# Performance work log

Measured on AMD Instinct MI355X. Metric: run time of the kernel, lower is better.

Reference implementation:

```python
import jax, jax.numpy as jnp
import numpy as np

D_MODEL = 512
NUM_FACTORS = 32
SCALE = D_MODEL ** 0.5


def setup_inputs() -> dict:
    key = jax.random.key(0)
    ks = jax.random.split(key, 12)
    B, T, TF = 64, 1024, 512
    s = 0.02
    return {
        "y_hat": jax.random.normal(ks[0], (B, T, D_MODEL), jnp.float32),
        "weather_hist": jax.random.normal(ks[1], (B, T, NUM_FACTORS), jnp.float32),
        "weather_fore": jax.random.normal(ks[2], (B, TF, NUM_FACTORS), jnp.float32),
        "Wq": jax.random.normal(ks[3], (D_MODEL, D_MODEL), jnp.float32) * s,
        "bq": jnp.zeros((D_MODEL,), jnp.float32),
        "Wk": jax.random.normal(ks[4], (NUM_FACTORS, D_MODEL), jnp.float32) * s,
        "bk": jnp.zeros((D_MODEL,), jnp.float32),
        "Wv": jax.random.normal(ks[5], (NUM_FACTORS, D_MODEL), jnp.float32) * s,
        "bv": jnp.zeros((D_MODEL,), jnp.float32),
        "Ws": jax.random.normal(ks[6], (D_MODEL, D_MODEL), jnp.float32) * s,
        "bs": jnp.zeros((D_MODEL,), jnp.float32),
    }


def reference(y_hat, weather_hist, weather_fore, Wq, bq, Wk, bk, Wv, bv, Ws, bs):
    # weather: [B, S, F] with S = T_hist + T_fore
    weather = jnp.concatenate([weather_hist, weather_fore], axis=1)
    Q = y_hat @ Wq + bq                         # [B, T, D]
    K = weather @ Wk + bk                       # [B, S, D]
    V = weather @ Wv + bv                       # [B, S, D]
    scores = jnp.einsum("btd,bsd->bts", Q, K) / SCALE
    attn = jax.nn.softmax(scores, axis=-1)      # [B, T, S]
    correction = jnp.einsum("bts,bsd->btd", attn, V)
    combined = correction @ Ws + bs             # [B, T, D]
    # pooled softmax gating over time
    logits = jnp.sum(combined * y_hat, axis=-1, keepdims=True) / SCALE  # [B, T, 1]
    P = jax.nn.softmax(logits, axis=1)
    final = jnp.sum(P * y_hat, axis=1, keepdims=True)  # [B, 1, D]
    return y_hat + final  # broadcast = expand_as
```

## Files before the change

kernel.cpp:

```cpp
#include <hip/hip_runtime.h>
#include <hip/hip_bf16.h>

typedef __bf16 bf16_t;
typedef bf16_t bf16x8 __attribute__((ext_vector_type(8)));
typedef bf16_t bf16x4 __attribute__((ext_vector_type(4)));
typedef float  floatx4 __attribute__((ext_vector_type(4)));

#define MFMA16(a,b,c) __builtin_amdgcn_mfma_f32_16x16x32_bf16((a),(b),(c),0,0,0)

constexpr float INV_SCALE = 0.04419417382415922f;

__device__ __forceinline__ bf16x8 load8(const void* p, size_t idx, int isbf) {
    if (isbf) return *(const bf16x8*)((const bf16_t*)p + idx);
    const floatx4* f = (const floatx4*)((const float*)p + idx);
    floatx4 a = f[0], b = f[1];
    bf16x8 r;
    r[0]=(bf16_t)a[0]; r[1]=(bf16_t)a[1]; r[2]=(bf16_t)a[2]; r[3]=(bf16_t)a[3];
    r[4]=(bf16_t)b[0]; r[5]=(bf16_t)b[1]; r[6]=(bf16_t)b[2]; r[7]=(bf16_t)b[3];
    return r;
}
__device__ __forceinline__ float loadf(const void* p, size_t idx, int isbf) {
    return isbf ? (float)((const bf16_t*)p)[idx] : ((const float*)p)[idx];
}

__global__ __launch_bounds__(256) void k_detect(
    const void* __restrict__ y, int* __restrict__ flag,
    const void* __restrict__ bq, const void* __restrict__ bv,
    const void* __restrict__ bs,
    float* __restrict__ bqf, float* __restrict__ bvf, float* __restrict__ bsf)
{
    __shared__ int cnt[4];
    const unsigned* w = (const unsigned*)y;
    unsigned x = w[threadIdx.x];
    unsigned e = (x >> 7) & 0xFFu;
    bool hit = (e >= 100u && e <= 141u);
    unsigned long long m = __ballot(hit);
    if ((threadIdx.x & 63) == 0) cnt[threadIdx.x >> 6] = __popcll(m);
    __syncthreads();
    int isbf = (cnt[0] + cnt[1] + cnt[2] + cnt[3]) >= 128;
    if (threadIdx.x == 0) *flag = isbf;
    for (int i = threadIdx.x; i < 512; i += 256) {
        bqf[i] = loadf(bq, i, isbf);
        bvf[i] = loadf(bv, i, isbf);
        bsf[i] = loadf(bs, i, isbf);
    }
}

__global__ __launch_bounds__(256) void k_wtrans(
    const void* __restrict__ Ws, bf16_t* __restrict__ WsT,
    const int* __restrict__ flag)
{
    int isbf = *flag;
    int idx = blockIdx.x * 256 + threadIdx.x;
    int k = idx >> 9, n = idx & 511;
    WsT[(size_t)n * 512 + k] = (bf16_t)loadf(Ws, idx, isbf);
}

__global__ __launch_bounds__(256) void k_m12(
    const void* __restrict__ Wq, const void* __restrict__ Wk,
    const void* __restrict__ Wv, const bf16_t* __restrict__ WsT,
    const float* __restrict__ bqf, const float* __restrict__ bvf,
    const float* __restrict__ bsf,
    bf16_t* __restrict__ M1, bf16_t* __restrict__ M2,
    float* __restrict__ b2, float* __restrict__ bqk,
    const int* __restrict__ flag)
{
    int isbf = *flag;
    if (blockIdx.x == 0) {
        int wave = threadIdx.x >> 6, lane = threadIdx.x & 63;
        int u = lane & 15, q = lane >> 4;
        int n0 = wave * 128;
        {
            floatx4 acc[2][8] = {};
            for (int ks = 0; ks < 16; ++ks) {
                bf16x8 a0 = load8(Wk, (size_t)u * 512 + ks * 32 + q * 8, isbf);
                bf16x8 a1 = load8(Wk, (size_t)(16 + u) * 512 + ks * 32 + q * 8, isbf);
#pragma unroll
                for (int nt = 0; nt < 8; ++nt) {
                    bf16x8 bb = load8(Wq, (size_t)(n0 + nt * 16 + u) * 512 + ks * 32 + q * 8, isbf);
                    acc[0][nt] = MFMA16(a0, bb, acc[0][nt]);
                    acc[1][nt] = MFMA16(a1, bb, acc[1][nt]);
                }
            }
#pragma unroll
            for (int mt = 0; mt < 2; ++mt)
#pragma unroll
                for (int nt = 0; nt < 8; ++nt)
#pragma unroll
                    for (int r = 0; r < 4; ++r)
                        M1[(size_t)(mt * 16 + q * 4 + r) * 512 + n0 + nt * 16 + u] =
                            (bf16_t)acc[mt][nt][r];
        }
        {
            floatx4 acc[2][8] = {};
            for (int ks = 0; ks < 16; ++ks) {
                bf16x8 a0 = load8(Wv, (size_t)u * 512 + ks * 32 + q * 8, isbf);
                bf16x8 a1 = load8(Wv, (size_t)(16 + u) * 512 + ks * 32 + q * 8, isbf);
#pragma unroll
                for (int nt = 0; nt < 8; ++nt) {
                    bf16x8 bb = *(const bf16x8*)(WsT + (size_t)(n0 + nt * 16 + u) * 512 + ks * 32 + q * 8);
                    acc[0][nt] = MFMA16(a0, bb, acc[0][nt]);
                    acc[1][nt] = MFMA16(a1, bb, acc[1][nt]);
                }
            }
#pragma unroll
            for (int mt = 0; mt < 2; ++mt)
#pragma unroll
                for (int nt = 0; nt < 8; ++nt)
#pragma unroll
                    for (int r = 0; r < 4; ++r)
                        M2[(size_t)(mt * 16 + q * 4 + r) * 512 + n0 + nt * 16 + u] =
                            (bf16_t)acc[mt][nt][r];
        }
    } else if (blockIdx.x <= 2) {
        int n = (blockIdx.x - 1) * 256 + threadIdx.x;
        float s = 0.f;
        for (int d = 0; d < 512; ++d) s += bvf[d] * (float)WsT[(size_t)n * 512 + d];
        b2[n] = s + bsf[n];
    } else {
        if (threadIdx.x < 32) {
            int f = threadIdx.x;
            float s = 0.f;
            for (int d = 0; d < 512; ++d) s += bqf[d] * loadf(Wk, (size_t)f * 512 + d, isbf);
            bqk[f] = s;
        }
    }
}

__global__ __launch_bounds__(256) void k_weather(
    const void* __restrict__ hist, const void* __restrict__ fore,
    bf16_t* __restrict__ Wb, bf16_t* __restrict__ WbT,
    const int* __restrict__ flag)
{
    __shared__ bf16_t tile[32][36];
    int isbf = *flag;
    int b = blockIdx.x / 48, st = blockIdx.x % 48;
    int s0 = st * 32;
    int sl = threadIdx.x >> 3, f0 = (threadIdx.x & 7) * 4;
    int s = s0 + sl;
    const void* sp; size_t src;
    if (s < 1024) { sp = hist; src = ((size_t)b * 1024 + s) * 32 + f0; }
    else          { sp = fore; src = ((size_t)b * 512 + (s - 1024)) * 32 + f0; }
    bf16x4 v;
    if (isbf) v = *(const bf16x4*)((const bf16_t*)sp + src);
    else {
        floatx4 fv = *(const floatx4*)((const float*)sp + src);
#pragma unroll
        for (int i = 0; i < 4; ++i) v[i] = (bf16_t)fv[i];
    }
    *(bf16x4*)(Wb + ((size_t)b * 1536 + s) * 32 + f0) = v;
#pragma unroll
    for (int i = 0; i < 4; ++i) tile[sl][f0 + i] = v[i];
    __syncthreads();
    int f = threadIdx.x >> 3, so = (threadIdx.x & 7) * 4;
    bf16x4 w;
#pragma unroll
    for (int i = 0; i < 4; ++i) w[i] = tile[so + i][f];
    *(bf16x4*)(WbT + ((size_t)b * 32 + f) * 1536 + s0 + so) = w;
}

__global__ __launch_bounds__(256) void k_qz(
    const void* __restrict__ Y, const bf16_t* __restrict__ M1,
    const bf16_t* __restrict__ M2, const float* __restrict__ bqk,
    const float* __restrict__ b2,
    bf16_t* __restrict__ Q2, float* __restrict__ Z, float* __restrict__ zb,
    const int* __restrict__ flag)
{
    int isbf = *flag;
    int wave = threadIdx.x >> 6, lane = threadIdx.x & 63;
    int u = lane & 15, q = lane >> 4;
    size_t r0 = (size_t)blockIdx.x * 64 + wave * 16;
    floatx4 accQ[2] = {}, accZ[2] = {};
    float zbp = 0.f;
    for (int ks = 0; ks < 16; ++ks) {
        bf16x8 a = load8(Y, (r0 + u) * 512 + ks * 32 + q * 8, isbf);
        const floatx4* bp = (const floatx4*)(b2 + ks * 32 + q * 8);
        floatx4 b2a = bp[0], b2b = bp[1];
#pragma unroll
        for (int j = 0; j < 4; ++j) zbp += (float)a[j] * b2a[j];
#pragma unroll
        for (int j = 0; j < 4; ++j) zbp += (float)a[4 + j] * b2b[j];
#pragma unroll
        for (int nt = 0; nt < 2; ++nt) {
            bf16x8 b1 = *(const bf16x8*)(M1 + (size_t)(nt * 16 + u) * 512 + ks * 32 + q * 8);
            bf16x8 b2v = *(const bf16x8*)(M2 + (size_t)(nt * 16 + u) * 512 + ks * 32 + q * 8);
            accQ[nt] = MFMA16(a, b1, accQ[nt]);
            accZ[nt] = MFMA16(a, b2v, accZ[nt]);
        }
    }
#pragma unroll
    for (int nt = 0; nt < 2; ++nt) {
        float bq_ = bqk[nt * 16 + u];
#pragma unroll
        for (int r = 0; r < 4; ++r) {
            size_t row = r0 + q * 4 + r;
            Q2[row * 32 + nt * 16 + u] = (bf16_t)(accQ[nt][r] + bq_);
            Z [row * 32 + nt * 16 + u] = accZ[nt][r];
        }
    }
    zbp += __shfl_xor(zbp, 16);
    zbp += __shfl_xor(zbp, 32);
    if (q == 0) zb[r0 + u] = zbp;
}

__global__ __launch_bounds__(256) void k_attn(
    const bf16_t* __restrict__ Wb, const bf16_t* __restrict__ WbT,
    const bf16_t* __restrict__ Q2, const float* __restrict__ Z,
    const float* __restrict__ zb, float* __restrict__ logits)
{
    __shared__ bf16_t P_lds[4][2][16][40];
    int wave = threadIdx.x >> 6, lane = threadIdx.x & 63;
    int u = lane & 15, q = lane >> 4;
    int b = blockIdx.x >> 4;
    int t0 = (blockIdx.x & 15) * 64 + wave * 16;
    const bf16_t* wbB = Wb  + (size_t)b * 1536 * 32;
    const bf16_t* wtB = WbT + (size_t)b * 32 * 1536;
    bf16x8 q2f = *(const bf16x8*)(Q2 + ((size_t)b * 1024 + t0 + u) * 32 + q * 8);
    floatx4 acc[2] = {};
    float l_acc = 0.f;
    const floatx4 z4 = {};
    for (int c = 0; c < 48; ++c) {
        int sB = c * 32, db = c & 1;
        bf16x8 a0  = *(const bf16x8*)(wbB + (size_t)(sB + u) * 32 + q * 8);
        bf16x8 a1  = *(const bf16x8*)(wbB + (size_t)(sB + 16 + u) * 32 + q * 8);
        bf16x8 wt0 = *(const bf16x8*)(wtB + (size_t)u * 1536 + sB + q * 8);
        bf16x8 wt1 = *(const bf16x8*)(wtB + (size_t)(16 + u) * 1536 + sB + q * 8);
        floatx4 st0 = MFMA16(a0, q2f, z4);
        floatx4 st1 = MFMA16(a1, q2f, z4);
        bf16x4 p0, p1;
#pragma unroll
        for (int r = 0; r < 4; ++r) {
            float e0 = __expf(st0[r] * INV_SCALE);
            float e1 = __expf(st1[r] * INV_SCALE);
            l_acc += e0 + e1;
            p0[r] = (bf16_t)e0; p1[r] = (bf16_t)e1;
        }
        *(bf16x4*)&P_lds[wave][db][u][q * 4]      = p0;
        *(bf16x4*)&P_lds[wave][db][u][16 + q * 4] = p1;
        bf16x8 pb = *(const bf16x8*)&P_lds[wave][db][u][q * 8];
        acc[0] = MFMA16(wt0, pb, acc[0]);
        acc[1] = MFMA16(wt1, pb, acc[1]);
    }
    float l1 = l_acc + __shfl_xor(l_acc, 16);
    float lf = l1 + __shfl_xor(l1, 32);
    const float* zp = Z + ((size_t)b * 1024 + t0 + u) * 32 + q * 4;
    floatx4 z0 = *(const floatx4*)zp;
    floatx4 z1 = *(const floatx4*)(zp + 16);
    float dp = 0.f;
#pragma unroll
    for (int r = 0; r < 4; ++r) dp += acc[0][r] * z0[r] + acc[1][r] * z1[r];
    float d1 = dp + __shfl_xor(dp, 16);
    float df = d1 + __shfl_xor(d1, 32);
    if (q == 0)
        logits[(size_t)b * 1024 + t0 + u] =
            (df / lf + zb[(size_t)b * 1024 + t0 + u]) * INV_SCALE;
}

__global__ __launch_bounds__(256) void k_finalout(
    const float* __restrict__ logits, const void* __restrict__ Y,
    void* __restrict__ out, const int* __restrict__ flag)
{
    __shared__ float P[1024];
    __shared__ float red[4];
    __shared__ float red2[4][64];
    __shared__ float ffin[64];
    __shared__ float s_max, s_sum;
    int isbf = *flag;
    int b = blockIdx.x >> 3, dc = blockIdx.x & 7;
    int tid = threadIdx.x, wid = tid >> 6;
    float l4[4];
#pragma unroll
    for (int i = 0; i < 4; ++i) l4[i] = logits[(size_t)b * 1024 + tid * 4 + i];
    float m = fmaxf(fmaxf(l4[0], l4[1]), fmaxf(l4[2], l4[3]));
#pragma unroll
    for (int off = 1; off < 64; off <<= 1) m = fmaxf(m, __shfl_xor(m, off));
    if ((tid & 63) == 0) red[wid] = m;
    __syncthreads();
    if (tid == 0) s_max = fmaxf(fmaxf(red[0], red[1]), fmaxf(red[2], red[3]));
    __syncthreads();
    float mx = s_max, ls = 0.f;
#pragma unroll
    for (int i = 0; i < 4; ++i) {
        float e = __expf(l4[i] - mx);
        P[tid * 4 + i] = e;
        ls += e;
    }
#pragma unroll
    for (int off = 1; off < 64; off <<= 1) ls += __shfl_xor(ls, off);
    if ((tid & 63) == 0) red[wid] = ls;
    __syncthreads();
    if (tid == 0) s_sum = red[0] + red[1] + red[2] + red[3];
    __syncthreads();
    int d = dc * 64 + (tid & 63), tg = tid >> 6;
    size_t ybase = (size_t)b * 1024 * 512;
    float acc = 0.f;
    for (int t = tg * 256; t < tg * 256 + 256; ++t)
        acc += P[t] * loadf(Y, ybase + (size_t)t * 512 + d, isbf);
    red2[tg][tid & 63] = acc;
    __syncthreads();
    if (tg == 0) ffin[tid] = (red2[0][tid] + red2[1][tid] + red2[2][tid] + red2[3][tid]) / s_sum;
    __syncthreads();
    float fv = ffin[tid & 63];
    if (isbf) {
        bf16_t* o = (bf16_t*)out; const bf16_t* y = (const bf16_t*)Y;
        for (int t = tg * 256; t < tg * 256 + 256; ++t) {
            size_t idx = ybase + (size_t)t * 512 + d;
            o[idx] = (bf16_t)((float)y[idx] + fv);
        }
    } else {
        float* o = (float*)out; const float* y = (const float*)Y;
        for (int t = tg * 256; t < tg * 256 + 256; ++t) {
            size_t idx = ybase + (size_t)t * 512 + d;
            o[idx] = y[idx] + fv;
        }
    }
}

extern "C" void kernel_launch(void* const* d_in, const int* in_sizes, int n_in,
                              void* d_out, int out_size, void* d_ws, size_t ws_size,
                              hipStream_t stream)
{
    const void* y_hat = d_in[0];
    const void* hist  = d_in[1];
    const void* fore  = d_in[2];
    const void* Wq    = d_in[3];
    const void* bq    = d_in[4];
    const void* Wk    = d_in[5];
    const void* Wv    = d_in[7];
    const void* bv    = d_in[8];
    const void* Ws    = d_in[9];
    const void* bs    = d_in[10];

    char* ws = (char*)d_ws;
    int*    flag   = (int*)   (ws);
    float*  bqf    = (float*) (ws + 16);
    float*  bvf    = (float*) (ws + 2064);
    float*  bsf    = (float*) (ws + 4112);
    float*  bqk    = (float*) (ws + 6160);
    float*  b2     = (float*) (ws + 6288);
    bf16_t* WsT    = (bf16_t*)(ws + 8336);
    bf16_t* M1     = (bf16_t*)(ws + 532624);
    bf16_t* M2     = (bf16_t*)(ws + 565392);
    bf16_t* Wb     = (bf16_t*)(ws + 598160);
    bf16_t* WbT    = (bf16_t*)(ws + 6889616);
    bf16_t* Q2     = (bf16_t*)(ws + 13181072);
    float*  Z      = (float*) (ws + 17375376);
    float*  zb     = (float*) (ws + 25763984);
    float*  logits = (float*) (ws + 26026128);

    k_detect  <<<1,    256, 0, stream>>>(y_hat, flag, bq, bv, bs, bqf, bvf, bsf);
    k_wtrans  <<<1024, 256, 0, stream>>>(Ws, WsT, flag);
    k_m12     <<<4,    256, 0, stream>>>(Wq, Wk, Wv, WsT, bqf, bvf, bsf,
                                         M1, M2, b2, bqk, flag);
    k_weather <<<3072, 256, 0, stream>>>(hist, fore, Wb, WbT, flag);
    k_qz      <<<1024, 256, 0, stream>>>(y_hat, M1, M2, bqk, b2, Q2, Z, zb, flag);
    k_attn    <<<1024, 256, 0, stream>>>(Wb, WbT, Q2, Z, zb, logits);
    k_finalout<<<512,  256, 0, stream>>>(logits, y_hat, d_out, flag);
}
```

Before: 536.0 us.

## Split pooling into parallel atomic reduce and vectorized output, inline dtype detection

Replaces the detect kernel and flag buffer with per-kernel wave-level dtype detection, tiles the Ws transpose through shared memory, and parallelizes bias precomputations. The final pooling is split into a 1024-block reduction that accumulates with float atomics and a separate fully coalesced vectorized add kernel. The attention grid is swizzled across batches. These target launch count, uncoalesced transpose writes, and the low-parallelism final output kernel, at the cost of an extra memset, atomics and a second full pass over y_hat.

```diff
diff --git a/kernel.cpp b/kernel.cpp
--- a/kernel.cpp
+++ b/kernel.cpp
@@ -5,10 +5,18 @@
 typedef bf16_t bf16x8 __attribute__((ext_vector_type(8)));
 typedef bf16_t bf16x4 __attribute__((ext_vector_type(4)));
 typedef float  floatx4 __attribute__((ext_vector_type(4)));
+typedef float  floatx2 __attribute__((ext_vector_type(2)));
 
 #define MFMA16(a,b,c) __builtin_amdgcn_mfma_f32_16x16x32_bf16((a),(b),(c),0,0,0)
 
 constexpr float INV_SCALE = 0.04419417382415922f;
+
+__device__ __forceinline__ int detect_isbf(const void* y) {
+    unsigned x = ((const unsigned*)y)[threadIdx.x & 63];
+    unsigned e = (x >> 7) & 0xFFu;
+    unsigned long long m = __ballot(e >= 100u && e <= 141u);
+    return __popcll(m) >= 32;
+}
 
 __device__ __forceinline__ bf16x8 load8(const void* p, size_t idx, int isbf) {
     if (isbf) return *(const bf16x8*)((const bf16_t*)p + idx);
@@ -23,51 +31,38 @@
     return isbf ? (float)((const bf16_t*)p)[idx] : ((const float*)p)[idx];
 }
 
-__global__ __launch_bounds__(256) void k_detect(
-    const void* __restrict__ y, int* __restrict__ flag,
+__global__ __launch_bounds__(256) void k_prep1(
+    const void* __restrict__ Ws, bf16_t* __restrict__ WsT,
+    const void* __restrict__ Y)
+{
+    __shared__ float t[32][33];
+    int isbf = detect_isbf(Y);
+    int ti = blockIdx.x >> 4, tj = blockIdx.x & 15;
+    int r = threadIdx.x >> 3, c0 = (threadIdx.x & 7) * 4;
+    size_t base = (size_t)(ti * 32 + r) * 512 + tj * 32 + c0;
+#pragma unroll
+    for (int i = 0; i < 4; ++i) t[r][c0 + i] = loadf(Ws, base + i, isbf);
+    __syncthreads();
+    bf16x4 v;
+#pragma unroll
+    for (int i = 0; i < 4; ++i) v[i] = (bf16_t)t[c0 + i][r];
+    *(bf16x4*)(WsT + (size_t)(tj * 32 + r) * 512 + ti * 32 + c0) = v;
+}
+
+__global__ __launch_bounds__(256) void k_prep2(
+    const void* __restrict__ Wq, const void* __restrict__ Wk,
+    const void* __restrict__ Wv, const void* __restrict__ Ws,
+    const bf16_t* __restrict__ WsT,
     const void* __restrict__ bq, const void* __restrict__ bv,
     const void* __restrict__ bs,
-    float* __restrict__ bqf, float* __restrict__ bvf, float* __restrict__ bsf)
-{
-    __shared__ int cnt[4];
-    const unsigned* w = (const unsigned*)y;
-    unsigned x = w[threadIdx.x];
-    unsigned e = (x >> 7) & 0xFFu;
-    bool hit = (e >= 100u && e <= 141u);
-    unsigned long long m = __ballot(hit);
-    if ((threadIdx.x & 63) == 0) cnt[threadIdx.x >> 6] = __popcll(m);
-    __syncthreads();
-    int isbf = (cnt[0] + cnt[1] + cnt[2] + cnt[3]) >= 128;
-    if (threadIdx.x == 0) *flag = isbf;
-    for (int i = threadIdx.x; i < 512; i += 256) {
-        bqf[i] = loadf(bq, i, isbf);
-        bvf[i] = loadf(bv, i, isbf);
-        bsf[i] = loadf(bs, i, isbf);
-    }
-}
-
-__global__ __launch_bounds__(256) void k_wtrans(
-    const void* __restrict__ Ws, bf16_t* __restrict__ WsT,
-    const int* __restrict__ flag)
-{
-    int isbf = *flag;
-    int idx = blockIdx.x * 256 + threadIdx.x;
-    int k = idx >> 9, n = idx & 511;
-    WsT[(size_t)n * 512 + k] = (bf16_t)loadf(Ws, idx, isbf);
-}
-
-__global__ __launch_bounds__(256) void k_m12(
-    const void* __restrict__ Wq, const void* __restrict__ Wk,
-    const void* __restrict__ Wv, const bf16_t* __restrict__ WsT,
-    const float* __restrict__ bqf, const float* __restrict__ bvf,
-    const float* __restrict__ bsf,
     bf16_t* __restrict__ M1, bf16_t* __restrict__ M2,
     float* __restrict__ b2, float* __restrict__ bqk,
-    const int* __restrict__ flag)
-{
-    int isbf = *flag;
+    const void* __restrict__ Y)
+{
+    int isbf = detect_isbf(Y);
+    int tid = threadIdx.x;
     if (blockIdx.x == 0) {
-        int wave = threadIdx.x >> 6, lane = threadIdx.x & 63;
+        int wave = tid >> 6, lane = tid & 63;
         int u = lane & 15, q = lane >> 4;
         int n0 = wave * 128;
         {
@@ -113,16 +108,25 @@
                             (bf16_t)acc[mt][nt][r];
         }
     } else if (blockIdx.x <= 2) {
-        int n = (blockIdx.x - 1) * 256 + threadIdx.x;
-        float s = 0.f;
-        for (int d = 0; d < 512; ++d) s += bvf[d] * (float)WsT[(size_t)n * 512 + d];
-        b2[n] = s + bsf[n];
+        int n = (blockIdx.x - 1) * 256 + tid;
+        float acc = 0.f;
+#pragma unroll 4
+        for (int d = 0; d < 512; ++d)
+            acc += loadf(bv, d, isbf) * loadf(Ws, (size_t)d * 512 + n, isbf);
+        b2[n] = acc + loadf(bs, n, isbf);
     } else {
-        if (threadIdx.x < 32) {
-            int f = threadIdx.x;
-            float s = 0.f;
-            for (int d = 0; d < 512; ++d) s += bqf[d] * loadf(Wk, (size_t)f * 512 + d, isbf);
-            bqk[f] = s;
+        int wv = tid >> 6, lane = tid & 63;
+        int d0 = lane * 8;
+#pragma unroll
+        for (int i = 0; i < 8; ++i) {
+            int f = wv * 8 + i;
+            float acc = 0.f;
+#pragma unroll
+            for (int j = 0; j < 8; ++j)
+                acc += loadf(bq, d0 + j, isbf) * loadf(Wk, (size_t)f * 512 + d0 + j, isbf);
+#pragma unroll
+            for (int off = 1; off < 64; off <<= 1) acc += __shfl_xor(acc, off);
+            if (lane == 0) bqk[f] = acc;
         }
     }
 }
@@ -130,10 +134,10 @@
 __global__ __launch_bounds__(256) void k_weather(
     const void* __restrict__ hist, const void* __restrict__ fore,
     bf16_t* __restrict__ Wb, bf16_t* __restrict__ WbT,
-    const int* __restrict__ flag)
+    const void* __restrict__ Y)
 {
     __shared__ bf16_t tile[32][36];
-    int isbf = *flag;
+    int isbf = detect_isbf(Y);
     int b = blockIdx.x / 48, st = blockIdx.x % 48;
     int s0 = st * 32;
     int sl = threadIdx.x >> 3, f0 = (threadIdx.x & 7) * 4;
@@ -163,10 +167,9 @@
     const void* __restrict__ Y, const bf16_t* __restrict__ M1,
     const bf16_t* __restrict__ M2, const float* __restrict__ bqk,
     const float* __restrict__ b2,
-    bf16_t* __restrict__ Q2, float* __restrict__ Z, float* __restrict__ zb,
-    const int* __restrict__ flag)
-{
-    int isbf = *flag;
+    bf16_t* __restrict__ Q2, float* __restrict__ Z, float* __restrict__ zb)
+{
+    int isbf = detect_isbf(Y);
     int wave = threadIdx.x >> 6, lane = threadIdx.x & 63;
     int u = lane & 15, q = lane >> 4;
     size_t r0 = (size_t)blockIdx.x * 64 + wave * 16;
@@ -211,8 +214,9 @@
     __shared__ bf16_t P_lds[4][2][16][40];
     int wave = threadIdx.x >> 6, lane = threadIdx.x & 63;
     int u = lane & 15, q = lane >> 4;
-    int b = blockIdx.x >> 4;
-    int t0 = (blockIdx.x & 15) * 64 + wave * 16;
+    int swz = ((blockIdx.x & 7) << 7) | (blockIdx.x >> 3);
+    int b = swz >> 4;
+    int t0 = (swz & 15) * 64 + wave * 16;
     const bf16_t* wbB = Wb  + (size_t)b * 1536 * 32;
     const bf16_t* wtB = WbT + (size_t)b * 32 * 1536;
     bf16x8 q2f = *(const bf16x8*)(Q2 + ((size_t)b * 1024 + t0 + u) * 32 + q * 8);
@@ -256,63 +260,81 @@
             (df / lf + zb[(size_t)b * 1024 + t0 + u]) * INV_SCALE;
 }
 
-__global__ __launch_bounds__(256) void k_finalout(
+__global__ __launch_bounds__(256) void k_pool(
     const float* __restrict__ logits, const void* __restrict__ Y,
-    void* __restrict__ out, const int* __restrict__ flag)
+    float* __restrict__ fin)
 {
     __shared__ float P[1024];
     __shared__ float red[4];
-    __shared__ float red2[4][64];
-    __shared__ float ffin[64];
-    __shared__ float s_max, s_sum;
-    int isbf = *flag;
-    int b = blockIdx.x >> 3, dc = blockIdx.x & 7;
-    int tid = threadIdx.x, wid = tid >> 6;
-    float l4[4];
-#pragma unroll
-    for (int i = 0; i < 4; ++i) l4[i] = logits[(size_t)b * 1024 + tid * 4 + i];
+    __shared__ float s_val;
+    int isbf = detect_isbf(Y);
+    int b = blockIdx.x >> 4, ts = blockIdx.x & 15;
+    int tid = threadIdx.x, wv = tid >> 6;
+    floatx4 l4 = *(const floatx4*)(logits + (size_t)b * 1024 + tid * 4);
     float m = fmaxf(fmaxf(l4[0], l4[1]), fmaxf(l4[2], l4[3]));
 #pragma unroll
     for (int off = 1; off < 64; off <<= 1) m = fmaxf(m, __shfl_xor(m, off));
-    if ((tid & 63) == 0) red[wid] = m;
-    __syncthreads();
-    if (tid == 0) s_max = fmaxf(fmaxf(red[0], red[1]), fmaxf(red[2], red[3]));
-    __syncthreads();
-    float mx = s_max, ls = 0.f;
-#pragma unroll
-    for (int i = 0; i < 4; ++i) {
-        float e = __expf(l4[i] - mx);
-        P[tid * 4 + i] = e;
-        ls += e;
-    }
+    if ((tid & 63) == 0) red[wv] = m;
+    __syncthreads();
+    if (tid == 0) s_val = fmaxf(fmaxf(red[0], red[1]), fmaxf(red[2], red[3]));
+    __syncthreads();
+    float mx = s_val, ls = 0.f;
+    floatx4 e;
+#pragma unroll
+    for (int i = 0; i < 4; ++i) { e[i] = __expf(l4[i] - mx); ls += e[i]; }
+    *(floatx4*)&P[tid * 4] = e;
 #pragma unroll
     for (int off = 1; off < 64; off <<= 1) ls += __shfl_xor(ls, off);
-    if ((tid & 63) == 0) red[wid] = ls;
-    __syncthreads();
-    if (tid == 0) s_sum = red[0] + red[1] + red[2] + red[3];
-    __syncthreads();
-    int d = dc * 64 + (tid & 63), tg = tid >> 6;
-    size_t ybase = (size_t)b * 1024 * 512;
-    float acc = 0.f;
-    for (int t = tg * 256; t < tg * 256 + 256; ++t)
-        acc += P[t] * loadf(Y, ybase + (size_t)t * 512 + d, isbf);
-    red2[tg][tid & 63] = acc;
-    __syncthreads();
-    if (tg == 0) ffin[tid] = (red2[0][tid] + red2[1][tid] + red2[2][tid] + red2[3][tid]) / s_sum;
-    __syncthreads();
-    float fv = ffin[tid & 63];
+    __syncthreads();
+    if ((tid & 63) == 0) red[wv] = ls;
+    __syncthreads();
+    if (tid == 0) s_val = red[0] + red[1] + red[2] + red[3];
+    __syncthreads();
+    float inv = 1.f / s_val;
+    int d = tid * 2;
+    size_t base = (size_t)b * 1024 * 512 + d;
+    float a0 = 0.f, a1 = 0.f;
+    int t0 = ts * 64;
+#pragma unroll 4
+    for (int t = t0; t < t0 + 64; ++t) {
+        float y0, y1;
+        size_t off = base + (size_t)t * 512;
+        if (isbf) {
+            y0 = (float)((const bf16_t*)Y)[off];
+            y1 = (float)((const bf16_t*)Y)[off + 1];
+        } else {
+            floatx2 v = *(const floatx2*)((const float*)Y + off);
+            y0 = v[0]; y1 = v[1];
+        }
+        float p = P[t];
+        a0 += p * y0; a1 += p * y1;
+    }
+    atomicAdd(&fin[b * 512 + d], a0 * inv);
+    atomicAdd(&fin[b * 512 + d + 1], a1 * inv);
+}
+
+__global__ __launch_bounds__(256) void k_out(
+    const void* __restrict__ Y, const float* __restrict__ fin,
+    void* __restrict__ out)
+{
+    int isbf = detect_isbf(Y);
+    size_t idx = ((size_t)blockIdx.x * 256 + threadIdx.x) * 8;
+    int d = (int)(idx & 511);
+    int b = (int)(idx >> 19);
+    const float* f = fin + b * 512 + d;
     if (isbf) {
-        bf16_t* o = (bf16_t*)out; const bf16_t* y = (const bf16_t*)Y;
-        for (int t = tg * 256; t < tg * 256 + 256; ++t) {
-            size_t idx = ybase + (size_t)t * 512 + d;
-            o[idx] = (bf16_t)((float)y[idx] + fv);
-        }
+        bf16x8 y = *(const bf16x8*)((const bf16_t*)Y + idx);
+        bf16x8 o;
+#pragma unroll
+        for (int j = 0; j < 8; ++j) o[j] = (bf16_t)((float)y[j] + f[j]);
+        *(bf16x8*)((bf16_t*)out + idx) = o;
     } else {
-        float* o = (float*)out; const float* y = (const float*)Y;
-        for (int t = tg * 256; t < tg * 256 + 256; ++t) {
-            size_t idx = ybase + (size_t)t * 512 + d;
-            o[idx] = y[idx] + fv;
-        }
+        const floatx4* yp = (const floatx4*)((const float*)Y + idx);
+        floatx4 y0 = yp[0], y1 = yp[1], o0, o1;
+#pragma unroll
+        for (int j = 0; j < 4; ++j) { o0[j] = y0[j] + f[j]; o1[j] = y1[j] + f[j + 4]; }
+        floatx4* op = (floatx4*)((float*)out + idx);
+        op[0] = o0; op[1] = o1;
     }
 }
 
@@ -332,28 +354,26 @@
     const void* bs    = d_in[10];
 
     char* ws = (char*)d_ws;
-    int*    flag   = (int*)   (ws);
-    float*  bqf    = (float*) (ws + 16);
-    float*  bvf    = (float*) (ws + 2064);
-    float*  bsf    = (float*) (ws + 4112);
-    float*  bqk    = (float*) (ws + 6160);
-    float*  b2     = (float*) (ws + 6288);
-    bf16_t* WsT    = (bf16_t*)(ws + 8336);
-    bf16_t* M1     = (bf16_t*)(ws + 532624);
-    bf16_t* M2     = (bf16_t*)(ws + 565392);
-    bf16_t* Wb     = (bf16_t*)(ws + 598160);
-    bf16_t* WbT    = (bf16_t*)(ws + 6889616);
-    bf16_t* Q2     = (bf16_t*)(ws + 13181072);
-    float*  Z      = (float*) (ws + 17375376);
-    float*  zb     = (float*) (ws + 25763984);
-    float*  logits = (float*) (ws + 26026128);
-
-    k_detect  <<<1,    256, 0, stream>>>(y_hat, flag, bq, bv, bs, bqf, bvf, bsf);
-    k_wtrans  <<<1024, 256, 0, stream>>>(Ws, WsT, flag);
-    k_m12     <<<4,    256, 0, stream>>>(Wq, Wk, Wv, WsT, bqf, bvf, bsf,
-                                         M1, M2, b2, bqk, flag);
-    k_weather <<<3072, 256, 0, stream>>>(hist, fore, Wb, WbT, flag);
-    k_qz      <<<1024, 256, 0, stream>>>(y_hat, M1, M2, bqk, b2, Q2, Z, zb, flag);
-    k_attn    <<<1024, 256, 0, stream>>>(Wb, WbT, Q2, Z, zb, logits);
-    k_finalout<<<512,  256, 0, stream>>>(logits, y_hat, d_out, flag);
-}
+    bf16_t* WsT    = (bf16_t*)(ws);
+    bf16_t* M1     = (bf16_t*)(ws + 524288);
+    bf16_t* M2     = (bf16_t*)(ws + 557056);
+    float*  bqk    = (float*) (ws + 589824);
+    float*  b2     = (float*) (ws + 589952);
+    bf16_t* Wb     = (bf16_t*)(ws + 592000);
+    bf16_t* WbT    = (bf16_t*)(ws + 6883456);
+    bf16_t* Q2     = (bf16_t*)(ws + 13174912);
+    float*  Z      = (float*) (ws + 17369216);
+    float*  zb     = (float*) (ws + 25757824);
+    float*  logits = (float*) (ws + 26019968);
+    float*  fin    = (float*) (ws + 26282112);
+
+    k_prep1  <<<256,  256, 0, stream>>>(Ws, WsT, y_hat);
+    k_prep2  <<<4,    256, 0, stream>>>(Wq, Wk, Wv, Ws, WsT, bq, bv, bs,
+                                        M1, M2, b2, bqk, y_hat);
+    k_weather<<<3072, 256, 0, stream>>>(hist, fore, Wb, WbT, y_hat);
+    k_qz     <<<1024, 256, 0, stream>>>(y_hat, M1, M2, bqk, b2, Q2, Z, zb);
+    k_attn   <<<1024, 256, 0, stream>>>(Wb, WbT, Q2, Z, zb, logits);
+    hipMemsetAsync(fin, 0, 64 * 512 * sizeof(float), stream);
+    k_pool   <<<1024, 256, 0, stream>>>(logits, y_hat, fin);
+    k_out    <<<16384, 256, 0, stream>>>(y_hat, fin, d_out);
+}
```

Measured after the change: 514.2 us. -4.1%, faster.
